# Performance work log

Measured on AMD Instinct MI355X. Metric: run time of the kernel, lower is better.

The kernel has to match this reference:

```python
import jax, jax.numpy as jnp
import numpy as np

D_MODEL = 1024
N_HEADS = 16
HEAD_DIM = D_MODEL // N_HEADS


def _rotary_tables(seq_len, dim):
    # sin/cos tables: (seq_len, dim//2)
    pos = jnp.arange(seq_len, dtype=jnp.float32)[:, None]
    freqs = 1.0 / 10000.0 ** (jnp.arange(0, dim, 2, dtype=jnp.float32) / dim)
    angles = pos * freqs
    return jnp.sin(angles), jnp.cos(angles)


def _apply_rotary(x, sin, cos):
    # x: (B, H, N, head_dim); sin/cos: (N, head_dim//2) broadcast over B,H
    d_half = x.shape[-1] // 2
    x1, x2 = x[..., :d_half], x[..., d_half:]
    return jnp.concatenate([x1 * cos - x2 * sin, x1 * sin + x2 * cos], axis=-1)


def setup_inputs() -> dict:
    key = jax.random.key(0)
    k_x, k_q, k_k, k_v, k_o = jax.random.split(key, 5)
    B, N = 4, 2048
    scale = 1.0 / np.sqrt(D_MODEL)
    return {
        "x": jax.random.normal(k_x, (B, N, D_MODEL), dtype=jnp.float32),
        "Wq": jax.random.normal(k_q, (D_MODEL, D_MODEL), dtype=jnp.float32) * scale,
        "Wk": jax.random.normal(k_k, (D_MODEL, D_MODEL), dtype=jnp.float32) * scale,
        "Wv": jax.random.normal(k_v, (D_MODEL, D_MODEL), dtype=jnp.float32) * scale,
        "Wo": jax.random.normal(k_o, (D_MODEL, D_MODEL), dtype=jnp.float32) * scale,
    }


def reference(x, Wq, Wk, Wv, Wo):
    B, N, _ = x.shape
    # nn.Linear(d, d, bias=False): y = x @ W.T ; view+transpose -> (B, H, N, hd)
    def proj(W):
        return jnp.einsum('bnd,ed->bne', x, W).reshape(B, N, N_HEADS, HEAD_DIM).transpose(0, 2, 1, 3)

    Q, K, V = proj(Wq), proj(Wk), proj(Wv)
    sin, cos = _rotary_tables(N, HEAD_DIM)
    Q = _apply_rotary(Q, sin, cos)
    K = _apply_rotary(K, sin, cos)

    # SDPA (non-causal, dropout=0): softmax(Q K^T / sqrt(hd)) V
    scores = jnp.einsum('bhqd,bhkd->bhqk', Q, K) / jnp.sqrt(jnp.asarray(HEAD_DIM, x.dtype))
    attn = jax.nn.softmax(scores, axis=-1)
    out = jnp.einsum('bhqk,bhkd->bhqd', attn, V)  # (B, H, N, hd)
    out = out.transpose(0, 2, 1, 3).reshape(B, N, D_MODEL)
    return jnp.einsum('bnd,ed->bne', out, Wo)
```

## Files before the change

### kernel.cpp

```cpp
#include <hip/hip_runtime.h>
#include <stdint.h>

#define SEQ    2048
#define DMODEL 1024
#define NHEADS 16
#define HDIM   64
#define BATCH  4
#define MTOT   (BATCH*SEQ)

typedef __attribute__((ext_vector_type(8)))  short s16x8;
typedef __attribute__((ext_vector_type(4)))  short s16x4;
typedef __attribute__((ext_vector_type(4)))  float f32x4;
typedef __attribute__((ext_vector_type(16))) float f32x16;

#define OFF_SIN  ((size_t)0)
#define OFF_COS  ((size_t)262144)
#define OFF_XHI  ((size_t)524288)
#define OFF_WQH  ((size_t)34078720)
#define OFF_WKH  ((size_t)38273024)
#define OFF_WVH  ((size_t)42467328)
#define OFF_WOH  ((size_t)46661632)
#define OFF_QR   ((size_t)50855936)
#define OFF_KR   ((size_t)67633152)
#define OFF_VT   ((size_t)84410368)
#define OFF_AHI  ((size_t)101187584)

#define QSCALE 0.18033688011112042f

__device__ __forceinline__ uint16_t f2bf(float f){
  union{float f;uint32_t u;}v; v.f=f;
  uint32_t r=v.u+0x7fffu+((v.u>>16)&1u);
  return (uint16_t)(r>>16);
}
__device__ __forceinline__ float bf2f(uint16_t u){
  union{uint32_t u;float f;}v; v.u=((uint32_t)u)<<16; return v.f;
}

__device__ __forceinline__ void async16(void* lds, const void* g){
  __builtin_amdgcn_global_load_lds(
    (const __attribute__((address_space(1))) void*)g,
    (__attribute__((address_space(3))) void*)lds, 16, 0, 0);
}

__device__ __forceinline__ float fexp2(float x){
#if __has_builtin(__builtin_amdgcn_exp2f)
  return __builtin_amdgcn_exp2f(x);
#else
  float r; asm("v_exp_f32 %0, %1" : "=v"(r) : "v"(x)); return r;
#endif
}
__device__ __forceinline__ float frcp(float x){
#if __has_builtin(__builtin_amdgcn_rcpf)
  return __builtin_amdgcn_rcpf(x);
#else
  float r; asm("v_rcp_f32 %0, %1" : "=v"(r) : "v"(x)); return r;
#endif
}
__device__ __forceinline__ void plswap(unsigned a, unsigned b, unsigned &o0, unsigned &o1){
#if __has_builtin(__builtin_amdgcn_permlane32_swap)
  auto r = __builtin_amdgcn_permlane32_swap(a, b, false, false);
  o0 = (unsigned)r[0]; o1 = (unsigned)r[1];
#else
  unsigned ax = (unsigned)__shfl_xor((int)a, 32, 64);
  unsigned bx = (unsigned)__shfl_xor((int)b, 32, 64);
  bool hi = (threadIdx.x & 32) != 0;
  o0 = hi ? bx : a;
  o1 = hi ? b  : ax;
#endif
}

__global__ __launch_bounds__(256) void rope_tables_k(float* __restrict__ st, float* __restrict__ ct){
  int i = blockIdx.x*256 + threadIdx.x;
  if (i >= SEQ*32) return;
  int n = i>>5, j = i&31;
  double freq = pow(10000.0, -(double)j/32.0);
  double ang = (double)n*freq;
  st[i] = (float)sin(ang);
  ct[i] = (float)cos(ang);
}

__global__ __launch_bounds__(256) void cvt_k(const float* __restrict__ src,
                                             uint16_t* __restrict__ hi, int n4){
  int i = blockIdx.x*256 + threadIdx.x;
  if (i>=n4) return;
  f32x4 v = *(const f32x4*)(src + (size_t)i*4);
  s16x4 vh;
  #pragma unroll
  for(int r=0;r<4;r++) vh[r] = (short)f2bf(v[r]);
  *(s16x4*)(hi + (size_t)i*4) = vh;
}

__global__ __launch_bounds__(256) void cvtw_k(const float* __restrict__ s0, const float* __restrict__ s1,
                                              const float* __restrict__ s2, const float* __restrict__ s3,
                                              uint16_t* __restrict__ d0, uint16_t* __restrict__ d1,
                                              uint16_t* __restrict__ d2, uint16_t* __restrict__ d3){
  int i = blockIdx.x*256 + threadIdx.x;
  int y = blockIdx.y;
  const float* s = y==0? s0 : y==1? s1 : y==2? s2 : s3;
  uint16_t*    d = y==0? d0 : y==1? d1 : y==2? d2 : d3;
  f32x4 v = *(const f32x4*)(s + (size_t)i*4);
  s16x4 vh;
  #pragma unroll
  for(int r=0;r<4;r++) vh[r] = (short)f2bf(v[r]);
  *(s16x4*)(d + (size_t)i*4) = vh;
}

__device__ __forceinline__ void gemm_mainloop64(
  const uint16_t* __restrict__ A, const uint16_t* __restrict__ B,
  int m0, int e0, char* lA, char* lB, f32x4 acc[4][4])
{
  const int t = threadIdx.x;
  const int lane = t & 63;
  const int wr = t>>7, wc = (t>>6)&1;
  const int lq = lane&15, lg = lane>>4;
  const int rowA = wr*64 + lq;
  const int rowB = wc*64 + lq;

  int dbyte[4], srow[4], sbyte[4];
  #pragma unroll
  for (int s=0;s<4;s++){
    int d = s*4096 + t*16;
    int r = d>>7, c = (d>>4)&7;
    dbyte[s]=d; srow[s]=r; sbyte[s]=(c ^ (r&7))*16;
  }
  int chh[2];
  #pragma unroll
  for (int kh=0;kh<2;kh++) chh[kh] = (((kh<<2)|lg) ^ (lq&7))*16;

  const char* Ab = (const char*)A;
  const char* Bb = (const char*)B;

  for (int k0=0; k0<DMODEL; k0+=64){
    #pragma unroll
    for (int s=0;s<4;s++){
      async16(lA + dbyte[s], Ab + (size_t)(m0+srow[s])*2048 + k0*2 + sbyte[s]);
      async16(lB + dbyte[s], Bb + (size_t)(e0+srow[s])*2048 + k0*2 + sbyte[s]);
    }
    __syncthreads();
    #pragma unroll
    for (int kh=0;kh<2;kh++){
      s16x8 af[4], bfr[4];
      #pragma unroll
      for (int mi=0;mi<4;mi++) af[mi]  = *(const s16x8*)(lA + (rowA+mi*16)*128 + chh[kh]);
      #pragma unroll
      for (int ni=0;ni<4;ni++) bfr[ni] = *(const s16x8*)(lB + (rowB+ni*16)*128 + chh[kh]);
      __builtin_amdgcn_s_setprio(1);
      #pragma unroll
      for (int mi=0;mi<4;mi++){
        #pragma unroll
        for (int ni=0;ni<4;ni++)
          acc[mi][ni] = __builtin_amdgcn_mfma_f32_16x16x32_bf16(af[mi], bfr[ni], acc[mi][ni],0,0,0);
      }
      __builtin_amdgcn_s_setprio(0);
    }
    __syncthreads();
  }
}

__global__ __launch_bounds__(256) void gemm_qkv_k(
  const uint16_t* __restrict__ Xh,
  const uint16_t* __restrict__ WqH, const uint16_t* __restrict__ WkH, const uint16_t* __restrict__ WvH,
  const float* __restrict__ st, const float* __restrict__ ct,
  uint16_t* __restrict__ Qr, uint16_t* __restrict__ Kr, uint16_t* __restrict__ Vt)
{
  __shared__ char lA[128*128], lB[128*128];
  int m0 = blockIdx.x*128;
  int cti = blockIdx.y;
  int seg = cti>>3;
  int e0 = (cti&7)*128;
  const uint16_t* W = seg==0? WqH : (seg==1? WkH : WvH);
  f32x4 acc[4][4];
  #pragma unroll
  for(int i=0;i<4;i++){
    #pragma unroll
    for(int j=0;j<4;j++) acc[i][j] = (f32x4){0.f,0.f,0.f,0.f};
  }
  gemm_mainloop64(Xh, W, m0, e0, lA, lB, acc);

  int t=threadIdx.x, lane=t&63, lq=lane&15, lg=lane>>4;
  int wr=t>>7, wc=(t>>6)&1;
  int eb = e0 + wc*64;
  int h = eb>>6;
  int rbase = m0 + wr*64 + lg*4;
  if (seg<2){
    uint16_t* O = seg==0? Qr:Kr;
    float qs = seg==0 ? QSCALE : 1.0f;
    #pragma unroll
    for(int mi=0;mi<4;mi++){
      #pragma unroll
      for(int ni=0;ni<2;ni++){
        int j = ni*16+lq;
        #pragma unroll
        for(int r=0;r<4;r++){
          int m = rbase + mi*16 + r;
          int b = m>>11, n = m&2047;
          float sv = st[n*32+j], cv = ct[n*32+j];
          float x1 = acc[mi][ni][r], x2 = acc[mi][ni+2][r];
          size_t base = ((size_t)((b*NHEADS+h)*SEQ + n))*HDIM;
          O[base + j]      = f2bf((x1*cv - x2*sv)*qs);
          O[base + j + 32] = f2bf((x1*sv + x2*cv)*qs);
        }
      }
    }
  } else {
    #pragma unroll
    for(int mi=0;mi<4;mi++){
      #pragma unroll
      for(int ni=0;ni<4;ni++){
        int dh = ni*16+lq;
        int m = rbase + mi*16;
        int b = m>>11, n = m&2047;
        s16x4 v;
        #pragma unroll
        for(int r=0;r<4;r++) v[r] = (short)f2bf(acc[mi][ni][r]);
        *(s16x4*)(Vt + ((size_t)((b*NHEADS+h)*HDIM + dh))*SEQ + n) = v;
      }
    }
  }
}

__global__ __launch_bounds__(256) void attn_k(
  const uint16_t* __restrict__ Qr, const uint16_t* __restrict__ Kr, const uint16_t* __restrict__ Vt,
  uint16_t* __restrict__ Ah)
{
  __shared__ uint16_t ldsK[3][64*64];
  __shared__ uint16_t ldsV[3][64*64];

  int bid = blockIdx.x;
  int w = (bid & 7)*128 + (bid >> 3);
  int bh = w >> 4, qt = w & 15;
  int tid = threadIdx.x;
  int wid = tid >> 6, lane = tid & 63;
  int l31 = lane & 31, hi = lane >> 5;
  int q0 = qt*128 + wid*32;

  const uint16_t* Qb = Qr + (size_t)bh*SEQ*HDIM;
  const uint16_t* Kb = Kr + (size_t)bh*SEQ*HDIM;
  const uint16_t* Vb = Vt + (size_t)bh*HDIM*SEQ;

  s16x8 qf[4];
  #pragma unroll
  for (int sp=0; sp<4; ++sp)
    qf[sp] = *(const s16x8*)(Qb + (size_t)(q0 + l31)*HDIM + sp*16 + hi*8);

  s16x8 ones;
  #pragma unroll
  for (int j=0;j<8;j++) ones[j] = (short)0x3F80;

  f32x16 zm16;
  #pragma unroll
  for (int r=0;r<16;r++) zm16[r] = -16.0f;

  f32x16 oa[2], lacc;
  #pragma unroll
  for (int r=0;r<16;r++){ oa[0][r]=0.f; oa[1][r]=0.f; lacc[r]=0.f; }

  auto STAGE = [&](int buf, int t){
    const char* Ks = (const char*)(Kb + (size_t)t*64*HDIM);
    char* dK = (char*)&ldsK[buf][0];
    char* dV = (char*)&ldsV[buf][0];
    #pragma unroll
    for (int r=0; r<2; ++r){
      int ci = r*256 + tid;
      int sc = ci ^ ((ci>>3)&7);
      async16(dK + ci*16, Ks + sc*16);
    }
    #pragma unroll
    for (int r=0; r<2; ++r){
      int ci = r*256 + tid;
      int row = ci>>3;
      int sc = (ci&7) ^ (row&7);
      async16(dV + ci*16, (const char*)Vb + ((size_t)row*SEQ + (size_t)t*64)*2 + sc*16);
    }
  };

  STAGE(0, 0);
  STAGE(1, 1);
  asm volatile("s_waitcnt vmcnt(4)" ::: "memory");
  __syncthreads();

  const int NT = SEQ/64;
  int cur = 0;
  for (int t=0; t<NT; ++t){
    int nxt2 = cur+2; if (nxt2>=3) nxt2-=3;
    if (t+2 < NT) STAGE(nxt2, t+2);
    const char* bK = (const char*)&ldsK[cur][0];
    const char* bV = (const char*)&ldsV[cur][0];

    s16x8 kf0[4], kf1[4];
    #pragma unroll
    for (int sp=0; sp<4; ++sp){
      int cc = (2*sp + hi) ^ (l31 & 7);
      kf0[sp] = *(const s16x8*)(bK + l31*128 + cc*16);
      kf1[sp] = *(const s16x8*)(bK + (32+l31)*128 + cc*16);
    }
    f32x16 sacc0 = zm16, sacc1 = zm16;
    __builtin_amdgcn_s_setprio(1);
    #pragma unroll
    for (int sp=0; sp<4; ++sp)
      sacc0 = __builtin_amdgcn_mfma_f32_32x32x16_bf16(kf0[sp], qf[sp], sacc0, 0,0,0);
    #pragma unroll
    for (int sp=0; sp<4; ++sp)
      sacc1 = __builtin_amdgcn_mfma_f32_32x32x16_bf16(kf1[sp], qf[sp], sacc1, 0,0,0);
    __builtin_amdgcn_s_setprio(0);

    s16x8 vf0[4];
    #pragma unroll
    for (int db=0; db<2; ++db)
      #pragma unroll
      for (int s=0; s<2; ++s){
        int cc = (2*s + hi) ^ (l31 & 7);
        vf0[db*2+s] = *(const s16x8*)(bV + (db*32+l31)*128 + cc*16);
      }

    float p[16];
    #pragma unroll
    for (int r=0;r<16;r++) p[r] = fexp2(sacc0[r]);
    uint32_t pw[8];
    #pragma unroll
    for (int j=0;j<8;j++)
      asm("v_cvt_pk_bf16_f32 %0, %1, %2" : "=v"(pw[j]) : "v"(p[2*j]), "v"(p[2*j+1]));
    unsigned w0,w1,w2,w3, x0,x1,x2,x3;
    plswap(pw[0], pw[2], w0, w2);
    plswap(pw[1], pw[3], w1, w3);
    plswap(pw[4], pw[6], x0, x2);
    plswap(pw[5], pw[7], x1, x3);
    union { uint32_t wd[4]; s16x8 v; } pa0, pa1;
    pa0.wd[0]=w0; pa0.wd[1]=w1; pa0.wd[2]=w2; pa0.wd[3]=w3;
    pa1.wd[0]=x0; pa1.wd[1]=x1; pa1.wd[2]=x2; pa1.wd[3]=x3;
    __builtin_amdgcn_s_setprio(1);
    #pragma unroll
    for (int db=0; db<2; ++db){
      oa[db] = __builtin_amdgcn_mfma_f32_32x32x16_bf16(pa0.v, vf0[db*2+0], oa[db], 0,0,0);
      oa[db] = __builtin_amdgcn_mfma_f32_32x32x16_bf16(pa1.v, vf0[db*2+1], oa[db], 0,0,0);
    }
    lacc = __builtin_amdgcn_mfma_f32_32x32x16_bf16(pa0.v, ones, lacc, 0,0,0);
    lacc = __builtin_amdgcn_mfma_f32_32x32x16_bf16(pa1.v, ones, lacc, 0,0,0);
    __builtin_amdgcn_s_setprio(0);

    s16x8 vf1[4];
    #pragma unroll
    for (int db=0; db<2; ++db)
      #pragma unroll
      for (int s=0; s<2; ++s){
        int cc = (4 + 2*s + hi) ^ (l31 & 7);
        vf1[db*2+s] = *(const s16x8*)(bV + (db*32+l31)*128 + cc*16);
      }

    #pragma unroll
    for (int r=0;r<16;r++) p[r] = fexp2(sacc1[r]);
    #pragma unroll
    for (int j=0;j<8;j++)
      asm("v_cvt_pk_bf16_f32 %0, %1, %2" : "=v"(pw[j]) : "v"(p[2*j]), "v"(p[2*j+1]));
    plswap(pw[0], pw[2], w0, w2);
    plswap(pw[1], pw[3], w1, w3);
    plswap(pw[4], pw[6], x0, x2);
    plswap(pw[5], pw[7], x1, x3);
    pa0.wd[0]=w0; pa0.wd[1]=w1; pa0.wd[2]=w2; pa0.wd[3]=w3;
    pa1.wd[0]=x0; pa1.wd[1]=x1; pa1.wd[2]=x2; pa1.wd[3]=x3;
    __builtin_amdgcn_s_setprio(1);
    #pragma unroll
    for (int db=0; db<2; ++db){
      oa[db] = __builtin_amdgcn_mfma_f32_32x32x16_bf16(pa0.v, vf1[db*2+0], oa[db], 0,0,0);
      oa[db] = __builtin_amdgcn_mfma_f32_32x32x16_bf16(pa1.v, vf1[db*2+1], oa[db], 0,0,0);
    }
    lacc = __builtin_amdgcn_mfma_f32_32x32x16_bf16(pa0.v, ones, lacc, 0,0,0);
    lacc = __builtin_amdgcn_mfma_f32_32x32x16_bf16(pa1.v, ones, lacc, 0,0,0);
    __builtin_amdgcn_s_setprio(0);

    if (t+2 < NT)      asm volatile("s_waitcnt vmcnt(4)" ::: "memory");
    else if (t+1 < NT) asm volatile("s_waitcnt vmcnt(0)" ::: "memory");
    if (t+1 < NT)      asm volatile("s_barrier" ::: "memory");
    cur = cur+1; if (cur>=3) cur-=3;
  }

  int b = bh >> 4, h = bh & 15;
  #pragma unroll
  for (int r=0;r<16;r++){
    int q = (r&3) + 8*(r>>2) + 4*hi;
    float inv = frcp(lacc[r]);
    size_t mrow = ((size_t)(b*SEQ + q0 + q))*DMODEL + (size_t)h*HDIM + l31;
    #pragma unroll
    for (int db=0; db<2; ++db)
      Ah[mrow + db*32] = f2bf(oa[db][r]*inv);
  }
}

__global__ __launch_bounds__(256) void gemm_out_k(
  const uint16_t* __restrict__ Ahp, const uint16_t* __restrict__ WoH, float* __restrict__ C)
{
  __shared__ char lA[128*128], lB[128*128];
  int m0 = blockIdx.x*128;
  int e0 = blockIdx.y*128;
  f32x4 acc[4][4];
  #pragma unroll
  for(int i=0;i<4;i++){
    #pragma unroll
    for(int j=0;j<4;j++) acc[i][j] = (f32x4){0.f,0.f,0.f,0.f};
  }
  gemm_mainloop64(Ahp, WoH, m0, e0, lA, lB, acc);
  int t=threadIdx.x, lane=t&63, lq=lane&15, lg=lane>>4;
  int wr=t>>7, wc=(t>>6)&1;
  int rbase = m0 + wr*64 + lg*4;
  int cb = e0 + wc*64;
  #pragma unroll
  for(int mi=0;mi<4;mi++){
    #pragma unroll
    for(int ni=0;ni<4;ni++){
      #pragma unroll
      for(int r=0;r<4;r++)
        C[(size_t)(rbase+mi*16+r)*DMODEL + cb + ni*16 + lq] = acc[mi][ni][r];
    }
  }
}

extern "C" void kernel_launch(void* const* d_in, const int* in_sizes, int n_in,
                              void* d_out, int out_size, void* d_ws, size_t ws_size,
                              hipStream_t stream) {
  const float* x  = (const float*)d_in[0];
  const float* Wq = (const float*)d_in[1];
  const float* Wk = (const float*)d_in[2];
  const float* Wv = (const float*)d_in[3];
  const float* Wo = (const float*)d_in[4];
  float* out = (float*)d_out;
  char* ws = (char*)d_ws;

  float* sin_t = (float*)(ws + OFF_SIN);
  float* cos_t = (float*)(ws + OFF_COS);
  uint16_t* xhi = (uint16_t*)(ws + OFF_XHI);
  uint16_t* wqh = (uint16_t*)(ws + OFF_WQH);
  uint16_t* wkh = (uint16_t*)(ws + OFF_WKH);
  uint16_t* wvh = (uint16_t*)(ws + OFF_WVH);
  uint16_t* woh = (uint16_t*)(ws + OFF_WOH);
  uint16_t* Qr  = (uint16_t*)(ws + OFF_QR);
  uint16_t* Kr  = (uint16_t*)(ws + OFF_KR);
  uint16_t* Vt  = (uint16_t*)(ws + OFF_VT);
  uint16_t* ahi = (uint16_t*)(ws + OFF_AHI);

  rope_tables_k<<<dim3(256),dim3(256),0,stream>>>(sin_t, cos_t);
  cvt_k<<<dim3(8192),dim3(256),0,stream>>>(x, xhi, (MTOT*DMODEL)/4);
  cvtw_k<<<dim3(1024,4),dim3(256),0,stream>>>(Wq, Wk, Wv, Wo, wqh, wkh, wvh, woh);

  gemm_qkv_k<<<dim3(MTOT/128, 24),dim3(256),0,stream>>>(xhi, wqh, wkh, wvh,
                                                        sin_t, cos_t, Qr, Kr, Vt);
  attn_k<<<dim3(BATCH*NHEADS*(SEQ/128)),dim3(256),0,stream>>>(Qr, Kr, Vt, ahi);
  gemm_out_k<<<dim3(MTOT/128, 8),dim3(256),0,stream>>>(ahi, woh, out);
}
```

Measured before the change: 204.5 us.

## Double query tile per wave in attention and switch to double-buffered K/V staging

Each wave now handles 64 query rows (two 32-row groups) instead of 32, so each K/V fragment read from LDS feeds twice as many MFMAs, and the grid is halved to 512 blocks of 256 queries. The K/V pipeline shrinks from a triple buffer with a two-tile lookahead to a double buffer with a one-tile lookahead, and each tile ends with a full vmcnt(0) wait and barrier. The intent is to cut LDS traffic and global K/V reloads per query. In exchange, register pressure rises from the duplicated accumulators and Q fragments, and there is less latency hiding and fewer blocks for occupancy.

```diff
diff --git a/kernel.cpp b/kernel.cpp
--- a/kernel.cpp
+++ b/kernel.cpp
@@ -223,25 +223,27 @@
   const uint16_t* __restrict__ Qr, const uint16_t* __restrict__ Kr, const uint16_t* __restrict__ Vt,
   uint16_t* __restrict__ Ah)
 {
-  __shared__ uint16_t ldsK[3][64*64];
-  __shared__ uint16_t ldsV[3][64*64];
+  __shared__ uint16_t ldsK[2][64*64];
+  __shared__ uint16_t ldsV[2][64*64];
 
   int bid = blockIdx.x;
-  int w = (bid & 7)*128 + (bid >> 3);
-  int bh = w >> 4, qt = w & 15;
+  int w = (bid & 7)*64 + (bid >> 3);
+  int bh = w >> 3, qt = w & 7;
   int tid = threadIdx.x;
   int wid = tid >> 6, lane = tid & 63;
   int l31 = lane & 31, hi = lane >> 5;
-  int q0 = qt*128 + wid*32;
+  int q0 = qt*256 + wid*64;
 
   const uint16_t* Qb = Qr + (size_t)bh*SEQ*HDIM;
   const uint16_t* Kb = Kr + (size_t)bh*SEQ*HDIM;
   const uint16_t* Vb = Vt + (size_t)bh*HDIM*SEQ;
 
-  s16x8 qf[4];
-  #pragma unroll
-  for (int sp=0; sp<4; ++sp)
-    qf[sp] = *(const s16x8*)(Qb + (size_t)(q0 + l31)*HDIM + sp*16 + hi*8);
+  s16x8 qfA[4], qfB[4];
+  #pragma unroll
+  for (int sp=0; sp<4; ++sp){
+    qfA[sp] = *(const s16x8*)(Qb + (size_t)(q0 + l31)*HDIM + sp*16 + hi*8);
+    qfB[sp] = *(const s16x8*)(Qb + (size_t)(q0 + 32 + l31)*HDIM + sp*16 + hi*8);
+  }
 
   s16x8 ones;
   #pragma unroll
@@ -251,9 +253,12 @@
   #pragma unroll
   for (int r=0;r<16;r++) zm16[r] = -16.0f;
 
-  f32x16 oa[2], lacc;
-  #pragma unroll
-  for (int r=0;r<16;r++){ oa[0][r]=0.f; oa[1][r]=0.f; lacc[r]=0.f; }
+  f32x16 oaA[2], oaB[2], laccA, laccB;
+  #pragma unroll
+  for (int r=0;r<16;r++){
+    oaA[0][r]=0.f; oaA[1][r]=0.f; oaB[0][r]=0.f; oaB[1][r]=0.f;
+    laccA[r]=0.f; laccB[r]=0.f;
+  }
 
   auto STAGE = [&](int buf, int t){
     const char* Ks = (const char*)(Kb + (size_t)t*64*HDIM);
@@ -275,114 +280,111 @@
   };
 
   STAGE(0, 0);
-  STAGE(1, 1);
-  asm volatile("s_waitcnt vmcnt(4)" ::: "memory");
+  asm volatile("s_waitcnt vmcnt(0)" ::: "memory");
   __syncthreads();
 
   const int NT = SEQ/64;
-  int cur = 0;
   for (int t=0; t<NT; ++t){
-    int nxt2 = cur+2; if (nxt2>=3) nxt2-=3;
-    if (t+2 < NT) STAGE(nxt2, t+2);
+    int cur = t & 1;
+    if (t+1 < NT) STAGE(cur^1, t+1);
     const char* bK = (const char*)&ldsK[cur][0];
     const char* bV = (const char*)&ldsV[cur][0];
-
-    s16x8 kf0[4], kf1[4];
-    #pragma unroll
-    for (int sp=0; sp<4; ++sp){
-      int cc = (2*sp + hi) ^ (l31 & 7);
-      kf0[sp] = *(const s16x8*)(bK + l31*128 + cc*16);
-      kf1[sp] = *(const s16x8*)(bK + (32+l31)*128 + cc*16);
-    }
-    f32x16 sacc0 = zm16, sacc1 = zm16;
-    __builtin_amdgcn_s_setprio(1);
-    #pragma unroll
-    for (int sp=0; sp<4; ++sp)
-      sacc0 = __builtin_amdgcn_mfma_f32_32x32x16_bf16(kf0[sp], qf[sp], sacc0, 0,0,0);
-    #pragma unroll
-    for (int sp=0; sp<4; ++sp)
-      sacc1 = __builtin_amdgcn_mfma_f32_32x32x16_bf16(kf1[sp], qf[sp], sacc1, 0,0,0);
-    __builtin_amdgcn_s_setprio(0);
-
-    s16x8 vf0[4];
-    #pragma unroll
-    for (int db=0; db<2; ++db)
-      #pragma unroll
-      for (int s=0; s<2; ++s){
-        int cc = (2*s + hi) ^ (l31 & 7);
-        vf0[db*2+s] = *(const s16x8*)(bV + (db*32+l31)*128 + cc*16);
-      }
-
-    float p[16];
-    #pragma unroll
-    for (int r=0;r<16;r++) p[r] = fexp2(sacc0[r]);
-    uint32_t pw[8];
-    #pragma unroll
-    for (int j=0;j<8;j++)
-      asm("v_cvt_pk_bf16_f32 %0, %1, %2" : "=v"(pw[j]) : "v"(p[2*j]), "v"(p[2*j+1]));
-    unsigned w0,w1,w2,w3, x0,x1,x2,x3;
-    plswap(pw[0], pw[2], w0, w2);
-    plswap(pw[1], pw[3], w1, w3);
-    plswap(pw[4], pw[6], x0, x2);
-    plswap(pw[5], pw[7], x1, x3);
-    union { uint32_t wd[4]; s16x8 v; } pa0, pa1;
-    pa0.wd[0]=w0; pa0.wd[1]=w1; pa0.wd[2]=w2; pa0.wd[3]=w3;
-    pa1.wd[0]=x0; pa1.wd[1]=x1; pa1.wd[2]=x2; pa1.wd[3]=x3;
-    __builtin_amdgcn_s_setprio(1);
+    #pragma unroll
+    for (int sub=0; sub<2; ++sub){
+      int krow = sub*32 + l31;
+      s16x8 kf[4];
+      #pragma unroll
+      for (int sp=0; sp<4; ++sp){
+        int cc = (2*sp + hi) ^ (l31 & 7);
+        kf[sp] = *(const s16x8*)(bK + krow*128 + cc*16);
+      }
+      f32x16 saccA = zm16, saccB = zm16;
+      __builtin_amdgcn_s_setprio(1);
+      #pragma unroll
+      for (int sp=0; sp<4; ++sp)
+        saccA = __builtin_amdgcn_mfma_f32_32x32x16_bf16(kf[sp], qfA[sp], saccA, 0,0,0);
+      #pragma unroll
+      for (int sp=0; sp<4; ++sp)
+        saccB = __builtin_amdgcn_mfma_f32_32x32x16_bf16(kf[sp], qfB[sp], saccB, 0,0,0);
+      __builtin_amdgcn_s_setprio(0);
+      s16x8 vf[4];
+      #pragma unroll
+      for (int db=0; db<2; ++db)
+        #pragma unroll
+        for (int s=0; s<2; ++s){
+          int cc = (4*sub + 2*s + hi) ^ (l31 & 7);
+          vf[db*2+s] = *(const s16x8*)(bV + (db*32+l31)*128 + cc*16);
+        }
+      {
+        float p[16];
+        #pragma unroll
+        for (int r=0;r<16;r++) p[r] = fexp2(saccA[r]);
+        uint32_t pw[8];
+        #pragma unroll
+        for (int j=0;j<8;j++)
+          asm("v_cvt_pk_bf16_f32 %0, %1, %2" : "=v"(pw[j]) : "v"(p[2*j]), "v"(p[2*j+1]));
+        unsigned w0,w1,w2,w3, x0,x1,x2,x3;
+        plswap(pw[0], pw[2], w0, w2);
+        plswap(pw[1], pw[3], w1, w3);
+        plswap(pw[4], pw[6], x0, x2);
+        plswap(pw[5], pw[7], x1, x3);
+        union { uint32_t wd[4]; s16x8 v; } pa0, pa1;
+        pa0.wd[0]=w0; pa0.wd[1]=w1; pa0.wd[2]=w2; pa0.wd[3]=w3;
+        pa1.wd[0]=x0; pa1.wd[1]=x1; pa1.wd[2]=x2; pa1.wd[3]=x3;
+        __builtin_amdgcn_s_setprio(1);
+        #pragma unroll
+        for (int db=0; db<2; ++db){
+          oaA[db] = __builtin_amdgcn_mfma_f32_32x32x16_bf16(pa0.v, vf[db*2+0], oaA[db], 0,0,0);
+          oaA[db] = __builtin_amdgcn_mfma_f32_32x32x16_bf16(pa1.v, vf[db*2+1], oaA[db], 0,0,0);
+        }
+        laccA = __builtin_amdgcn_mfma_f32_32x32x16_bf16(pa0.v, ones, laccA, 0,0,0);
+        laccA = __builtin_amdgcn_mfma_f32_32x32x16_bf16(pa1.v, ones, laccA, 0,0,0);
+        __builtin_amdgcn_s_setprio(0);
+      }
+      {
+        float p[16];
+        #pragma unroll
+        for (int r=0;r<16;r++) p[r] = fexp2(saccB[r]);
+        uint32_t pw[8];
+        #pragma unroll
+        for (int j=0;j<8;j++)
+          asm("v_cvt_pk_bf16_f32 %0, %1, %2" : "=v"(pw[j]) : "v"(p[2*j]), "v"(p[2*j+1]));
+        unsigned w0,w1,w2,w3, x0,x1,x2,x3;
+        plswap(pw[0], pw[2], w0, w2);
+        plswap(pw[1], pw[3], w1, w3);
+        plswap(pw[4], pw[6], x0, x2);
+        plswap(pw[5], pw[7], x1, x3);
+        union { uint32_t wd[4]; s16x8 v; } pa0, pa1;
+        pa0.wd[0]=w0; pa0.wd[1]=w1; pa0.wd[2]=w2; pa0.wd[3]=w3;
+        pa1.wd[0]=x0; pa1.wd[1]=x1; pa1.wd[2]=x2; pa1.wd[3]=x3;
+        __builtin_amdgcn_s_setprio(1);
+        #pragma unroll
+        for (int db=0; db<2; ++db){
+          oaB[db] = __builtin_amdgcn_mfma_f32_32x32x16_bf16(pa0.v, vf[db*2+0], oaB[db], 0,0,0);
+          oaB[db] = __builtin_amdgcn_mfma_f32_32x32x16_bf16(pa1.v, vf[db*2+1], oaB[db], 0,0,0);
+        }
+        laccB = __builtin_amdgcn_mfma_f32_32x32x16_bf16(pa0.v, ones, laccB, 0,0,0);
+        laccB = __builtin_amdgcn_mfma_f32_32x32x16_bf16(pa1.v, ones, laccB, 0,0,0);
+        __builtin_amdgcn_s_setprio(0);
+      }
+    }
+    asm volatile("s_waitcnt vmcnt(0)" ::: "memory");
+    __syncthreads();
+  }
+
+  int b = bh >> 4, h = bh & 15;
+  #pragma unroll
+  for (int r=0;r<16;r++){
+    int qoff = (r&3) + 8*(r>>2) + 4*hi;
+    float invA = frcp(laccA[r]);
+    float invB = frcp(laccB[r]);
+    size_t mrowA = ((size_t)(b*SEQ + q0 + qoff))*DMODEL + (size_t)h*HDIM + l31;
+    size_t mrowB = ((size_t)(b*SEQ + q0 + 32 + qoff))*DMODEL + (size_t)h*HDIM + l31;
     #pragma unroll
     for (int db=0; db<2; ++db){
-      oa[db] = __builtin_amdgcn_mfma_f32_32x32x16_bf16(pa0.v, vf0[db*2+0], oa[db], 0,0,0);
-      oa[db] = __builtin_amdgcn_mfma_f32_32x32x16_bf16(pa1.v, vf0[db*2+1], oa[db], 0,0,0);
-    }
-    lacc = __builtin_amdgcn_mfma_f32_32x32x16_bf16(pa0.v, ones, lacc, 0,0,0);
-    lacc = __builtin_amdgcn_mfma_f32_32x32x16_bf16(pa1.v, ones, lacc, 0,0,0);
-    __builtin_amdgcn_s_setprio(0);
-
-    s16x8 vf1[4];
-    #pragma unroll
-    for (int db=0; db<2; ++db)
-      #pragma unroll
-      for (int s=0; s<2; ++s){
-        int cc = (4 + 2*s + hi) ^ (l31 & 7);
-        vf1[db*2+s] = *(const s16x8*)(bV + (db*32+l31)*128 + cc*16);
-      }
-
-    #pragma unroll
-    for (int r=0;r<16;r++) p[r] = fexp2(sacc1[r]);
-    #pragma unroll
-    for (int j=0;j<8;j++)
-      asm("v_cvt_pk_bf16_f32 %0, %1, %2" : "=v"(pw[j]) : "v"(p[2*j]), "v"(p[2*j+1]));
-    plswap(pw[0], pw[2], w0, w2);
-    plswap(pw[1], pw[3], w1, w3);
-    plswap(pw[4], pw[6], x0, x2);
-    plswap(pw[5], pw[7], x1, x3);
-    pa0.wd[0]=w0; pa0.wd[1]=w1; pa0.wd[2]=w2; pa0.wd[3]=w3;
-    pa1.wd[0]=x0; pa1.wd[1]=x1; pa1.wd[2]=x2; pa1.wd[3]=x3;
-    __builtin_amdgcn_s_setprio(1);
-    #pragma unroll
-    for (int db=0; db<2; ++db){
-      oa[db] = __builtin_amdgcn_mfma_f32_32x32x16_bf16(pa0.v, vf1[db*2+0], oa[db], 0,0,0);
-      oa[db] = __builtin_amdgcn_mfma_f32_32x32x16_bf16(pa1.v, vf1[db*2+1], oa[db], 0,0,0);
-    }
-    lacc = __builtin_amdgcn_mfma_f32_32x32x16_bf16(pa0.v, ones, lacc, 0,0,0);
-    lacc = __builtin_amdgcn_mfma_f32_32x32x16_bf16(pa1.v, ones, lacc, 0,0,0);
-    __builtin_amdgcn_s_setprio(0);
-
-    if (t+2 < NT)      asm volatile("s_waitcnt vmcnt(4)" ::: "memory");
-    else if (t+1 < NT) asm volatile("s_waitcnt vmcnt(0)" ::: "memory");
-    if (t+1 < NT)      asm volatile("s_barrier" ::: "memory");
-    cur = cur+1; if (cur>=3) cur-=3;
-  }
-
-  int b = bh >> 4, h = bh & 15;
-  #pragma unroll
-  for (int r=0;r<16;r++){
-    int q = (r&3) + 8*(r>>2) + 4*hi;
-    float inv = frcp(lacc[r]);
-    size_t mrow = ((size_t)(b*SEQ + q0 + q))*DMODEL + (size_t)h*HDIM + l31;
-    #pragma unroll
-    for (int db=0; db<2; ++db)
-      Ah[mrow + db*32] = f2bf(oa[db][r]*inv);
+      Ah[mrowA + db*32] = f2bf(oaA[db][r]*invA);
+      Ah[mrowB + db*32] = f2bf(oaB[db][r]*invB);
+    }
   }
 }
 
@@ -443,6 +445,6 @@
 
   gemm_qkv_k<<<dim3(MTOT/128, 24),dim3(256),0,stream>>>(xhi, wqh, wkh, wvh,
                                                         sin_t, cos_t, Qr, Kr, Vt);
-  attn_k<<<dim3(BATCH*NHEADS*(SEQ/128)),dim3(256),0,stream>>>(Qr, Kr, Vt, ahi);
+  attn_k<<<dim3(BATCH*NHEADS*(SEQ/256)),dim3(256),0,stream>>>(Qr, Kr, Vt, ahi);
   gemm_out_k<<<dim3(MTOT/128, 8),dim3(256),0,stream>>>(ahi, woh, out);
 }
```

Result: slower. 219.0 us (+7.1%).
